# Optimization experiments

Hardware: AMD Instinct MI355X
Metric: run time of the kernel (lower is better)

Reference implementation:

```python
import jax, jax.numpy as jnp
import numpy as np

N_NODES = 100000
N_EDGES = 1600000
IN_CH = 3
HID = 32
BN_EPS = 1e-5


def setup_inputs() -> dict:
    key = jax.random.key(0)
    k_x, k_e1, k_e2, k_w, k_b, k_p = jax.random.split(key, 6)
    x = jax.random.normal(k_x, (N_NODES, IN_CH), dtype=jnp.float32)
    src = jax.random.randint(k_e1, (N_EDGES,), 0, N_NODES)
    dst = jax.random.randint(k_e2, (N_EDGES,), 0, N_NODES)
    edge_index = jnp.stack([src, dst]).astype(jnp.int64)
    # GCNConv linear params (glorot-ish init)
    W = jax.random.normal(k_w, (IN_CH, HID), dtype=jnp.float32) / np.sqrt(IN_CH)
    b = jnp.zeros((HID,), dtype=jnp.float32)
    bn_gamma = jnp.ones((HID,), dtype=jnp.float32)
    bn_beta = jnp.zeros((HID,), dtype=jnp.float32)
    prelu_w = jnp.full((1,), 0.25, dtype=jnp.float32)  # torch PReLU default
    return {"x": x, "edge_index": edge_index, "W": W, "b": b,
            "bn_gamma": bn_gamma, "bn_beta": bn_beta, "prelu_w": prelu_w}


def reference(x, edge_index, W, b, bn_gamma, bn_beta, prelu_w):
    src, dst = edge_index[0], edge_index[1]
    n = x.shape[0]
    # --- GCNConv: sym-normalized aggregation with self-loops ---
    # degree including self loop (edge weights = 1)
    deg = 1.0 + jax.ops.segment_sum(jnp.ones_like(src, dtype=x.dtype), dst,
                                    num_segments=n)
    dinv = jax.lax.rsqrt(deg)                       # deg^{-1/2}, [N]
    h = x @ W                                       # [N, HID]
    norm = dinv[src] * dinv[dst]                    # [E]
    msg = h[src] * norm[:, None]                    # [E, HID] gather
    agg = jax.ops.segment_sum(msg, dst, num_segments=n)  # scatter-add
    agg = agg + h * (1.0 / deg)[:, None]            # self-loop term
    agg = agg + b
    # --- BatchNorm1d (training-mode batch statistics, biased var) ---
    mean = jnp.mean(agg, axis=0)
    var = jnp.mean(jnp.square(agg - mean), axis=0)
    xhat = (agg - mean) * jax.lax.rsqrt(var + BN_EPS)
    y = xhat * bn_gamma + bn_beta
    # --- PReLU (single shared slope) ---
    y = jnp.where(y >= 0, y, prelu_w[0] * y)
    # dropout(p=0.5) is identity in eval / deterministic reference
    return y
```

## Files before the change

kernel.cpp:

```cpp
#include <hip/hip_runtime.h>

#define N_NODES 100000
#define N_EDGES 1600000
#define HID 32
#define BN_EPS 1e-5f

#define EPB   4096
#define NBLK  391
#define BSZ   512
#define NBUCK 196
#define SRC_MASK 0x1FFFFu


__global__ void bin_kernel(const int* __restrict__ src, const int* __restrict__ dst,
                           unsigned* __restrict__ bbuf, int* __restrict__ blen,
                           int* __restrict__ boffs) {
    __shared__ int hist[NBUCK], offs[NBUCK], curs[NBUCK];
    __shared__ int sc[256];
    __shared__ unsigned stage[EPB];
    int tid = threadIdx.x, blk = blockIdx.x;
    int e0 = blk * EPB;
    int cnt = N_EDGES - e0; if (cnt > EPB) cnt = EPB;

    unsigned pk[EPB / 256];
    int bk[EPB / 256];
#pragma unroll
    for (int i = 0; i < EPB / 256; ++i) {
        int j = tid + i * 256;
        if (j < cnt) {
            int e = e0 + j;
            int s = src[e], d = dst[e];
            bk[i] = d >> 9;
            pk[i] = ((unsigned)(d & (BSZ - 1)) << 17) | (unsigned)s;
        } else bk[i] = -1;
    }
    for (int j = tid; j < NBUCK; j += 256) hist[j] = 0;
    __syncthreads();
#pragma unroll
    for (int i = 0; i < EPB / 256; ++i)
        if (bk[i] >= 0) atomicAdd(&hist[bk[i]], 1);
    __syncthreads();
    int h = (tid < NBUCK) ? hist[tid] : 0;
    sc[tid] = h;
    __syncthreads();
    for (int off = 1; off < 256; off <<= 1) {
        int v = (tid >= off) ? sc[tid - off] : 0;
        __syncthreads();
        sc[tid] += v;
        __syncthreads();
    }
    if (tid < NBUCK) { offs[tid] = sc[tid] - h; curs[tid] = sc[tid] - h; }
    __syncthreads();
#pragma unroll
    for (int i = 0; i < EPB / 256; ++i)
        if (bk[i] >= 0) {
            int p = atomicAdd(&curs[bk[i]], 1);
            stage[p] = pk[i];
        }
    __syncthreads();
    for (int j = tid; j < cnt; j += 256) bbuf[e0 + j] = stage[j];
    for (int j = tid; j < NBUCK; j += 256) {
        blen[j * NBLK + blk]  = hist[j];
        boffs[j * NBLK + blk] = e0 + offs[j];
    }
}

__global__ void degxd_kernel(const unsigned* __restrict__ bbuf, const int* __restrict__ blen,
                             const int* __restrict__ boffs, const float* __restrict__ x,
                             float4* __restrict__ xd) {
    __shared__ int hist[BSZ];
    int tid = threadIdx.x, b = blockIdx.x;
    for (int j = tid; j < BSZ; j += 512) hist[j] = 0;
    __syncthreads();
    for (int r = tid; r < NBLK; r += 512) {
        int len = blen[b * NBLK + r];
        int off = boffs[b * NBLK + r];
        for (int k = 0; k < len; ++k) {
            unsigned p = bbuf[off + k];
            atomicAdd(&hist[p >> 17], 1);
        }
    }
    __syncthreads();
    int base = b << 9;
    for (int l = tid; l < BSZ; l += 512) {
        int n = base + l;
        if (n < N_NODES) {
            float rd = rsqrtf(1.0f + (float)hist[l]);
            xd[n] = make_float4(x[3 * n] * rd, x[3 * n + 1] * rd, x[3 * n + 2] * rd, rd);
        }
    }
}

__global__ void accum_kernel(const unsigned* __restrict__ bbuf, const int* __restrict__ blen,
                             const int* __restrict__ boffs, const float4* __restrict__ xd,
                             float4* __restrict__ S4, float* __restrict__ stats) {
    __shared__ float S[BSZ * 3];
    __shared__ float ls[8][9];
    int tid = threadIdx.x, b = blockIdx.x;
    for (int j = tid; j < BSZ * 3; j += 512) S[j] = 0.f;
    __syncthreads();
    for (int r = tid; r < NBLK; r += 512) {
        int len = blen[b * NBLK + r];
        int off = boffs[b * NBLK + r];
        for (int k = 0; k < len; ++k) {
            unsigned p = bbuf[off + k];
            float4 v = xd[p & SRC_MASK];
            int l3 = (int)(p >> 17) * 3;
            atomicAdd(&S[l3 + 0], v.x);
            atomicAdd(&S[l3 + 1], v.y);
            atomicAdd(&S[l3 + 2], v.z);
        }
    }
    __syncthreads();
    int base = b << 9;
    float st[9];
#pragma unroll
    for (int q = 0; q < 9; ++q) st[q] = 0.f;
    for (int l = tid; l < BSZ; l += 512) {
        int n = base + l;
        if (n < N_NODES) {
            float4 self = xd[n];
            float sx = S[l * 3 + 0] + self.x;
            float sy = S[l * 3 + 1] + self.y;
            float sz = S[l * 3 + 2] + self.z;
            S4[n] = make_float4(sx, sy, sz, self.w);
            float ax = self.w * sx, ay = self.w * sy, az = self.w * sz;
            st[0] += ax; st[1] += ay; st[2] += az;
            st[3] += ax * ax; st[4] += ax * ay; st[5] += ax * az;
            st[6] += ay * ay; st[7] += ay * az; st[8] += az * az;
        }
    }
    for (int m = 1; m < 64; m <<= 1)
#pragma unroll
        for (int q = 0; q < 9; ++q) st[q] += __shfl_xor(st[q], m);
    int wave = tid >> 6;
    if ((tid & 63) == 0)
#pragma unroll
        for (int q = 0; q < 9; ++q) ls[wave][q] = st[q];
    __syncthreads();
    if (tid < 9) {
        float s = 0.f;
#pragma unroll
        for (int w = 0; w < 8; ++w) s += ls[w][tid];
        atomicAdd(&stats[tid], s);
    }
}

__global__ void finalize_kernel(const float* __restrict__ stats, const float* __restrict__ W,
                                const float* __restrict__ b, const float* __restrict__ gamma,
                                const float* __restrict__ beta, float* __restrict__ cbuf) {
    int c = threadIdx.x;
    if (c >= HID) return;
    float m1x = stats[0], m1y = stats[1], m1z = stats[2];
    float Mxx = stats[3], Mxy = stats[4], Mxz = stats[5];
    float Myy = stats[6], Myz = stats[7], Mzz = stats[8];
    float w0 = W[c], w1 = W[HID + c], w2 = W[2 * HID + c];
    const float invn = 1.0f / (float)N_NODES;
    float m1w = m1x * w0 + m1y * w1 + m1z * w2;
    float mean = m1w * invn + b[c];
    float quad = w0 * w0 * Mxx + w1 * w1 * Myy + w2 * w2 * Mzz
               + 2.f * (w0 * w1 * Mxy + w0 * w2 * Mxz + w1 * w2 * Myz);
    float ex2 = quad * invn + 2.f * b[c] * m1w * invn + b[c] * b[c];
    float var = ex2 - mean * mean;
    float inv = rsqrtf(var + BN_EPS);
    float sc = gamma[c] * inv;
    float sh = beta[c] - mean * sc;
    cbuf[c] = w0 * sc;
    cbuf[HID + c] = w1 * sc;
    cbuf[2 * HID + c] = w2 * sc;
    cbuf[3 * HID + c] = b[c] * sc + sh;
}

__global__ void final_out_kernel(const float4* __restrict__ S4, const float* __restrict__ cbuf,
                                 const float* __restrict__ prelu, float* __restrict__ out) {
    int t = blockIdx.x * blockDim.x + threadIdx.x;
    if (t >= N_NODES * HID) return;
    int n = t >> 5, c = t & 31;
    float4 s = S4[n];
    float y = s.w * (s.x * cbuf[c] + s.y * cbuf[HID + c] + s.z * cbuf[2 * HID + c])
            + cbuf[3 * HID + c];
    float a = prelu[0];
    out[t] = y >= 0.f ? y : a * y;
}


__global__ void fb_count_kernel(const int* __restrict__ dst, int* __restrict__ cnt) {
    int e = blockIdx.x * blockDim.x + threadIdx.x;
    if (e < N_EDGES) atomicAdd(&cnt[dst[e]], 1);
}

__global__ void fb_xd_kernel(const float* __restrict__ x, const int* __restrict__ cnt,
                             float4* __restrict__ xd, float4* __restrict__ S4) {
    int n = blockIdx.x * blockDim.x + threadIdx.x;
    if (n >= N_NODES) return;
    float rd = rsqrtf(1.0f + (float)cnt[n]);
    float4 v = make_float4(x[3 * n] * rd, x[3 * n + 1] * rd, x[3 * n + 2] * rd, rd);
    xd[n] = v;
    S4[n] = v;
}

__global__ void fb_scatter_kernel(const int* __restrict__ src, const int* __restrict__ dst,
                                  const float4* __restrict__ xd, float4* __restrict__ S4) {
    int e = blockIdx.x * blockDim.x + threadIdx.x;
    if (e >= N_EDGES) return;
    int s = src[e], d = dst[e];
    float4 v = xd[s];
    float* p = (float*)&S4[d];
    atomicAdd(p + 0, v.x);
    atomicAdd(p + 1, v.y);
    atomicAdd(p + 2, v.z);
}

__global__ void fb_stats_kernel(const float4* __restrict__ S4, float* __restrict__ stats) {
    __shared__ float ls[4][9];
    int tid = threadIdx.x;
    int n = blockIdx.x * blockDim.x + tid;
    float st[9];
#pragma unroll
    for (int q = 0; q < 9; ++q) st[q] = 0.f;
    if (n < N_NODES) {
        float4 s = S4[n];
        float ax = s.w * s.x, ay = s.w * s.y, az = s.w * s.z;
        st[0] = ax; st[1] = ay; st[2] = az;
        st[3] = ax * ax; st[4] = ax * ay; st[5] = ax * az;
        st[6] = ay * ay; st[7] = ay * az; st[8] = az * az;
    }
    for (int m = 1; m < 64; m <<= 1)
#pragma unroll
        for (int q = 0; q < 9; ++q) st[q] += __shfl_xor(st[q], m);
    int wave = tid >> 6;
    if ((tid & 63) == 0)
#pragma unroll
        for (int q = 0; q < 9; ++q) ls[wave][q] = st[q];
    __syncthreads();
    if (tid < 9) {
        float s = ls[0][tid] + ls[1][tid] + ls[2][tid] + ls[3][tid];
        atomicAdd(&stats[tid], s);
    }
}


extern "C" void kernel_launch(void* const* d_in, const int* in_sizes, int n_in,
                              void* d_out, int out_size, void* d_ws, size_t ws_size,
                              hipStream_t stream) {
    const float* x     = (const float*)d_in[0];
    const int*   ei    = (const int*)d_in[1];
    const float* W     = (const float*)d_in[2];
    const float* b     = (const float*)d_in[3];
    const float* gamma = (const float*)d_in[4];
    const float* beta  = (const float*)d_in[5];
    const float* prelu = (const float*)d_in[6];

    const int* src = ei;
    const int* dst = ei + N_EDGES;
    char* ws = (char*)d_ws;
    float* out = (float*)d_out;

    const size_t NEEDED = 10219872;

    if (ws_size >= NEEDED) {
        float*    stats = (float*)(ws);
        float*    cbuf  = (float*)(ws + 64);
        unsigned* bbuf  = (unsigned*)(ws + 640);
        int*      blen  = (int*)(ws + 6406784);
        int*      boffs = (int*)(ws + 6713328);
        float4*   xd    = (float4*)(ws + 7019872);
        float4*   S4    = (float4*)(ws + 8619872);

        hipMemsetAsync(stats, 0, 64, stream);
        bin_kernel<<<NBLK, 256, 0, stream>>>(src, dst, bbuf, blen, boffs);
        degxd_kernel<<<NBUCK, 512, 0, stream>>>(bbuf, blen, boffs, x, xd);
        accum_kernel<<<NBUCK, 512, 0, stream>>>(bbuf, blen, boffs, xd, S4, stats);
        finalize_kernel<<<1, 64, 0, stream>>>(stats, W, b, gamma, beta, cbuf);
        final_out_kernel<<<(N_NODES * HID + 255) / 256, 256, 0, stream>>>(S4, cbuf, prelu, out);
    } else {
        int*    cnt   = (int*)(ws);
        float*  stats = (float*)(ws + 400000);
        float*  cbuf  = (float*)(ws + 400064);
        float4* xd    = (float4*)(ws + 400640);
        float4* S4    = (float4*)(ws + 2000640);

        hipMemsetAsync(ws, 0, 400064, stream);
        fb_count_kernel<<<(N_EDGES + 255) / 256, 256, 0, stream>>>(dst, cnt);
        fb_xd_kernel<<<(N_NODES + 255) / 256, 256, 0, stream>>>(x, cnt, xd, S4);
        fb_scatter_kernel<<<(N_EDGES + 255) / 256, 256, 0, stream>>>(src, dst, xd, S4);
        fb_stats_kernel<<<(N_NODES + 255) / 256, 256, 0, stream>>>(S4, stats);
        finalize_kernel<<<1, 64, 0, stream>>>(stats, W, b, gamma, beta, cbuf);
        final_out_kernel<<<(N_NODES * HID + 255) / 256, 256, 0, stream>>>(S4, cbuf, prelu, out);
    }
}
```

Before: 142.9 us.

## Split bucket degree and accumulation work across 8 blocks per bucket

The degree-count and accumulation kernels previously gave each destination bucket one 512-thread block. In that block each thread walked a whole source-block run serially, giving only 196 blocks and long sequential loops. Now each bucket is split into 8 groups of runs, with wave-per-run and lane-strided edge processing. Partial results are merged into global counts and S4 with global atomics. This adds separate xd and stats kernels plus extra global atomic traffic and launches, in exchange for much higher parallelism and coalesced bbuf reads.

Result: slower. 169.8 us (+18.8%).

```diff
diff --git a/kernel.cpp b/kernel.cpp
--- a/kernel.cpp
+++ b/kernel.cpp
@@ -10,6 +10,8 @@
 #define BSZ   512
 #define NBUCK 196
 #define SRC_MASK 0x1FFFFu
+#define GSPL  8
+#define RPB   ((NBLK + GSPL - 1) / GSPL)
 
 
 __global__ void bin_kernel(const int* __restrict__ src, const int* __restrict__ dst,
@@ -65,44 +67,57 @@
     }
 }
 
-__global__ void degxd_kernel(const unsigned* __restrict__ bbuf, const int* __restrict__ blen,
-                             const int* __restrict__ boffs, const float* __restrict__ x,
-                             float4* __restrict__ xd) {
+__global__ void deg_kernel(const unsigned* __restrict__ bbuf, const int* __restrict__ blen,
+                           const int* __restrict__ boffs, int* __restrict__ cnt) {
     __shared__ int hist[BSZ];
-    int tid = threadIdx.x, b = blockIdx.x;
-    for (int j = tid; j < BSZ; j += 512) hist[j] = 0;
-    __syncthreads();
-    for (int r = tid; r < NBLK; r += 512) {
+    int tid = threadIdx.x;
+    int b = blockIdx.x >> 3;
+    int g = blockIdx.x & 7;
+    for (int j = tid; j < BSZ; j += 256) hist[j] = 0;
+    __syncthreads();
+    int wave = tid >> 6, lane = tid & 63;
+    int r0 = g * RPB;
+    int r1 = r0 + RPB; if (r1 > NBLK) r1 = NBLK;
+    for (int r = r0 + wave; r < r1; r += 4) {
         int len = blen[b * NBLK + r];
         int off = boffs[b * NBLK + r];
-        for (int k = 0; k < len; ++k) {
-            unsigned p = bbuf[off + k];
-            atomicAdd(&hist[p >> 17], 1);
-        }
+        for (int k = lane; k < len; k += 64)
+            atomicAdd(&hist[bbuf[off + k] >> 17], 1);
     }
     __syncthreads();
     int base = b << 9;
-    for (int l = tid; l < BSZ; l += 512) {
-        int n = base + l;
-        if (n < N_NODES) {
-            float rd = rsqrtf(1.0f + (float)hist[l]);
-            xd[n] = make_float4(x[3 * n] * rd, x[3 * n + 1] * rd, x[3 * n + 2] * rd, rd);
-        }
-    }
+    for (int l = tid; l < BSZ; l += 256) {
+        int h = hist[l];
+        if (h && base + l < N_NODES) atomicAdd(&cnt[base + l], h);
+    }
+}
+
+__global__ void xd_kernel(const float* __restrict__ x, const int* __restrict__ cnt,
+                          float4* __restrict__ xd, float4* __restrict__ S4) {
+    int n = blockIdx.x * blockDim.x + threadIdx.x;
+    if (n >= N_NODES) return;
+    float rd = rsqrtf(1.0f + (float)cnt[n]);
+    float4 v = make_float4(x[3 * n] * rd, x[3 * n + 1] * rd, x[3 * n + 2] * rd, rd);
+    xd[n] = v;
+    S4[n] = v;
 }
 
 __global__ void accum_kernel(const unsigned* __restrict__ bbuf, const int* __restrict__ blen,
                              const int* __restrict__ boffs, const float4* __restrict__ xd,
-                             float4* __restrict__ S4, float* __restrict__ stats) {
+                             float4* __restrict__ S4) {
     __shared__ float S[BSZ * 3];
-    __shared__ float ls[8][9];
-    int tid = threadIdx.x, b = blockIdx.x;
-    for (int j = tid; j < BSZ * 3; j += 512) S[j] = 0.f;
-    __syncthreads();
-    for (int r = tid; r < NBLK; r += 512) {
+    int tid = threadIdx.x;
+    int b = blockIdx.x >> 3;
+    int g = blockIdx.x & 7;
+    for (int j = tid; j < BSZ * 3; j += 256) S[j] = 0.f;
+    __syncthreads();
+    int wave = tid >> 6, lane = tid & 63;
+    int r0 = g * RPB;
+    int r1 = r0 + RPB; if (r1 > NBLK) r1 = NBLK;
+    for (int r = r0 + wave; r < r1; r += 4) {
         int len = blen[b * NBLK + r];
         int off = boffs[b * NBLK + r];
-        for (int k = 0; k < len; ++k) {
+        for (int k = lane; k < len; k += 64) {
             unsigned p = bbuf[off + k];
             float4 v = xd[p & SRC_MASK];
             int l3 = (int)(p >> 17) * 3;
@@ -113,22 +128,33 @@
     }
     __syncthreads();
     int base = b << 9;
-    float st[9];
-#pragma unroll
-    for (int q = 0; q < 9; ++q) st[q] = 0.f;
-    for (int l = tid; l < BSZ; l += 512) {
+    for (int l = tid; l < BSZ; l += 256) {
         int n = base + l;
         if (n < N_NODES) {
-            float4 self = xd[n];
-            float sx = S[l * 3 + 0] + self.x;
-            float sy = S[l * 3 + 1] + self.y;
-            float sz = S[l * 3 + 2] + self.z;
-            S4[n] = make_float4(sx, sy, sz, self.w);
-            float ax = self.w * sx, ay = self.w * sy, az = self.w * sz;
-            st[0] += ax; st[1] += ay; st[2] += az;
-            st[3] += ax * ax; st[4] += ax * ay; st[5] += ax * az;
-            st[6] += ay * ay; st[7] += ay * az; st[8] += az * az;
+            float sx = S[l * 3 + 0], sy = S[l * 3 + 1], sz = S[l * 3 + 2];
+            if (sx != 0.f || sy != 0.f || sz != 0.f) {
+                float* p = (float*)&S4[n];
+                atomicAdd(p + 0, sx);
+                atomicAdd(p + 1, sy);
+                atomicAdd(p + 2, sz);
+            }
         }
+    }
+}
+
+__global__ void stats_kernel(const float4* __restrict__ S4, float* __restrict__ stats) {
+    __shared__ float ls[4][9];
+    int tid = threadIdx.x;
+    int n = blockIdx.x * blockDim.x + tid;
+    float st[9];
+#pragma unroll
+    for (int q = 0; q < 9; ++q) st[q] = 0.f;
+    if (n < N_NODES) {
+        float4 s = S4[n];
+        float ax = s.w * s.x, ay = s.w * s.y, az = s.w * s.z;
+        st[0] = ax; st[1] = ay; st[2] = az;
+        st[3] = ax * ax; st[4] = ax * ay; st[5] = ax * az;
+        st[6] = ay * ay; st[7] = ay * az; st[8] = az * az;
     }
     for (int m = 1; m < 64; m <<= 1)
 #pragma unroll
@@ -139,9 +165,7 @@
         for (int q = 0; q < 9; ++q) ls[wave][q] = st[q];
     __syncthreads();
     if (tid < 9) {
-        float s = 0.f;
-#pragma unroll
-        for (int w = 0; w < 8; ++w) s += ls[w][tid];
+        float s = ls[0][tid] + ls[1][tid] + ls[2][tid] + ls[3][tid];
         atomicAdd(&stats[tid], s);
     }
 }
@@ -189,16 +213,6 @@
     if (e < N_EDGES) atomicAdd(&cnt[dst[e]], 1);
 }
 
-__global__ void fb_xd_kernel(const float* __restrict__ x, const int* __restrict__ cnt,
-                             float4* __restrict__ xd, float4* __restrict__ S4) {
-    int n = blockIdx.x * blockDim.x + threadIdx.x;
-    if (n >= N_NODES) return;
-    float rd = rsqrtf(1.0f + (float)cnt[n]);
-    float4 v = make_float4(x[3 * n] * rd, x[3 * n + 1] * rd, x[3 * n + 2] * rd, rd);
-    xd[n] = v;
-    S4[n] = v;
-}
-
 __global__ void fb_scatter_kernel(const int* __restrict__ src, const int* __restrict__ dst,
                                   const float4* __restrict__ xd, float4* __restrict__ S4) {
     int e = blockIdx.x * blockDim.x + threadIdx.x;
@@ -211,34 +225,6 @@
     atomicAdd(p + 2, v.z);
 }
 
-__global__ void fb_stats_kernel(const float4* __restrict__ S4, float* __restrict__ stats) {
-    __shared__ float ls[4][9];
-    int tid = threadIdx.x;
-    int n = blockIdx.x * blockDim.x + tid;
-    float st[9];
-#pragma unroll
-    for (int q = 0; q < 9; ++q) st[q] = 0.f;
-    if (n < N_NODES) {
-        float4 s = S4[n];
-        float ax = s.w * s.x, ay = s.w * s.y, az = s.w * s.z;
-        st[0] = ax; st[1] = ay; st[2] = az;
-        st[3] = ax * ax; st[4] = ax * ay; st[5] = ax * az;
-        st[6] = ay * ay; st[7] = ay * az; st[8] = az * az;
-    }
-    for (int m = 1; m < 64; m <<= 1)
-#pragma unroll
-        for (int q = 0; q < 9; ++q) st[q] += __shfl_xor(st[q], m);
-    int wave = tid >> 6;
-    if ((tid & 63) == 0)
-#pragma unroll
-        for (int q = 0; q < 9; ++q) ls[wave][q] = st[q];
-    __syncthreads();
-    if (tid < 9) {
-        float s = ls[0][tid] + ls[1][tid] + ls[2][tid] + ls[3][tid];
-        atomicAdd(&stats[tid], s);
-    }
-}
-
 
 extern "C" void kernel_launch(void* const* d_in, const int* in_sizes, int n_in,
                               void* d_out, int out_size, void* d_ws, size_t ws_size,
@@ -256,21 +242,24 @@
     char* ws = (char*)d_ws;
     float* out = (float*)d_out;
 
-    const size_t NEEDED = 10219872;
+    const size_t NEEDED = 10619872;
 
     if (ws_size >= NEEDED) {
-        float*    stats = (float*)(ws);
-        float*    cbuf  = (float*)(ws + 64);
-        unsigned* bbuf  = (unsigned*)(ws + 640);
-        int*      blen  = (int*)(ws + 6406784);
-        int*      boffs = (int*)(ws + 6713328);
-        float4*   xd    = (float4*)(ws + 7019872);
-        float4*   S4    = (float4*)(ws + 8619872);
-
-        hipMemsetAsync(stats, 0, 64, stream);
+        int*      cnt   = (int*)(ws);
+        float*    stats = (float*)(ws + 400000);
+        float*    cbuf  = (float*)(ws + 400064);
+        unsigned* bbuf  = (unsigned*)(ws + 400640);
+        int*      blen  = (int*)(ws + 6806784);
+        int*      boffs = (int*)(ws + 7113328);
+        float4*   xd    = (float4*)(ws + 7419872);
+        float4*   S4    = (float4*)(ws + 9019872);
+
+        hipMemsetAsync(ws, 0, 400064, stream);
         bin_kernel<<<NBLK, 256, 0, stream>>>(src, dst, bbuf, blen, boffs);
-        degxd_kernel<<<NBUCK, 512, 0, stream>>>(bbuf, blen, boffs, x, xd);
-        accum_kernel<<<NBUCK, 512, 0, stream>>>(bbuf, blen, boffs, xd, S4, stats);
+        deg_kernel<<<NBUCK * GSPL, 256, 0, stream>>>(bbuf, blen, boffs, cnt);
+        xd_kernel<<<(N_NODES + 255) / 256, 256, 0, stream>>>(x, cnt, xd, S4);
+        accum_kernel<<<NBUCK * GSPL, 256, 0, stream>>>(bbuf, blen, boffs, xd, S4);
+        stats_kernel<<<(N_NODES + 255) / 256, 256, 0, stream>>>(S4, stats);
         finalize_kernel<<<1, 64, 0, stream>>>(stats, W, b, gamma, beta, cbuf);
         final_out_kernel<<<(N_NODES * HID + 255) / 256, 256, 0, stream>>>(S4, cbuf, prelu, out);
     } else {
@@ -282,9 +271,9 @@
 
         hipMemsetAsync(ws, 0, 400064, stream);
         fb_count_kernel<<<(N_EDGES + 255) / 256, 256, 0, stream>>>(dst, cnt);
-        fb_xd_kernel<<<(N_NODES + 255) / 256, 256, 0, stream>>>(x, cnt, xd, S4);
+        xd_kernel<<<(N_NODES + 255) / 256, 256, 0, stream>>>(x, cnt, xd, S4);
         fb_scatter_kernel<<<(N_EDGES + 255) / 256, 256, 0, stream>>>(src, dst, xd, S4);
-        fb_stats_kernel<<<(N_NODES + 255) / 256, 256, 0, stream>>>(S4, stats);
+        stats_kernel<<<(N_NODES + 255) / 256, 256, 0, stream>>>(S4, stats);
         finalize_kernel<<<1, 64, 0, stream>>>(stats, W, b, gamma, beta, cbuf);
         final_out_kernel<<<(N_NODES * HID + 255) / 256, 256, 0, stream>>>(S4, cbuf, prelu, out);
     }
```

## Compact bucketed edges into contiguous per-bucket arrays and fuse finalize into output

Applied to the files above, without the earlier changes.

Adds two prefix-scan kernels and a scatter pass that copy each destination bucket's edge runs into one contiguous array, folding the degree histogram and xd computation into that pass. The accumulate kernel then streams a contiguous range with 1024 threads instead of having each thread walk one variable-length run serially. This targets the poor parallelism and uncoalesced reads of the old per-run loops. The BN finalize is folded into a grid-stride output kernel so one launch is removed, at the cost of extra workspace, an extra copy of the edge buffer and two small scan launches.

After: 147.5 us. 3.3% more time.

```diff
diff --git a/kernel.cpp b/kernel.cpp
--- a/kernel.cpp
+++ b/kernel.cpp
@@ -13,7 +13,7 @@
 
 
 __global__ void bin_kernel(const int* __restrict__ src, const int* __restrict__ dst,
-                           unsigned* __restrict__ bbuf, int* __restrict__ blen,
+                           unsigned* __restrict__ staged, int* __restrict__ blen,
                            int* __restrict__ boffs) {
     __shared__ int hist[NBUCK], offs[NBUCK], curs[NBUCK];
     __shared__ int sc[256];
@@ -22,165 +22,203 @@
     int e0 = blk * EPB;
     int cnt = N_EDGES - e0; if (cnt > EPB) cnt = EPB;
 
-    unsigned pk[EPB / 256];
-    int bk[EPB / 256];
-#pragma unroll
-    for (int i = 0; i < EPB / 256; ++i) {
-        int j = tid + i * 256;
+    unsigned pk[8]; int bk[8];
+#pragma unroll
+    for (int i = 0; i < 8; ++i) {
+        int j = tid + i * 512;
         if (j < cnt) {
             int e = e0 + j;
-            int s = src[e], d = dst[e];
+            int d = dst[e];
             bk[i] = d >> 9;
-            pk[i] = ((unsigned)(d & (BSZ - 1)) << 17) | (unsigned)s;
+            pk[i] = ((unsigned)(d & (BSZ - 1)) << 17) | (unsigned)src[e];
         } else bk[i] = -1;
     }
-    for (int j = tid; j < NBUCK; j += 256) hist[j] = 0;
-    __syncthreads();
-#pragma unroll
-    for (int i = 0; i < EPB / 256; ++i)
+    for (int j = tid; j < NBUCK; j += 512) hist[j] = 0;
+    __syncthreads();
+#pragma unroll
+    for (int i = 0; i < 8; ++i)
         if (bk[i] >= 0) atomicAdd(&hist[bk[i]], 1);
     __syncthreads();
     int h = (tid < NBUCK) ? hist[tid] : 0;
-    sc[tid] = h;
+    if (tid < 256) sc[tid] = h;
     __syncthreads();
     for (int off = 1; off < 256; off <<= 1) {
-        int v = (tid >= off) ? sc[tid - off] : 0;
-        __syncthreads();
-        sc[tid] += v;
-        __syncthreads();
-    }
-    if (tid < NBUCK) { offs[tid] = sc[tid] - h; curs[tid] = sc[tid] - h; }
-    __syncthreads();
-#pragma unroll
-    for (int i = 0; i < EPB / 256; ++i)
+        int v = 0;
+        if (tid < 256 && tid >= off) v = sc[tid - off];
+        __syncthreads();
+        if (tid < 256) sc[tid] += v;
+        __syncthreads();
+    }
+    if (tid < NBUCK) { int ex = sc[tid] - h; offs[tid] = ex; curs[tid] = ex; }
+    __syncthreads();
+#pragma unroll
+    for (int i = 0; i < 8; ++i)
         if (bk[i] >= 0) {
             int p = atomicAdd(&curs[bk[i]], 1);
             stage[p] = pk[i];
         }
     __syncthreads();
-    for (int j = tid; j < cnt; j += 256) bbuf[e0 + j] = stage[j];
-    for (int j = tid; j < NBUCK; j += 256) {
+    for (int j = tid; j < cnt; j += 512) staged[e0 + j] = stage[j];
+    for (int j = tid; j < NBUCK; j += 512) {
         blen[j * NBLK + blk]  = hist[j];
         boffs[j * NBLK + blk] = e0 + offs[j];
     }
 }
 
-__global__ void degxd_kernel(const unsigned* __restrict__ bbuf, const int* __restrict__ blen,
-                             const int* __restrict__ boffs, const float* __restrict__ x,
-                             float4* __restrict__ xd) {
+__global__ void scan1_kernel(const int* __restrict__ blen, int* __restrict__ runoff,
+                             int* __restrict__ tot) {
+    __shared__ int sc[512];
+    int tid = threadIdx.x, b = blockIdx.x;
+    int v = (tid < NBLK) ? blen[b * NBLK + tid] : 0;
+    sc[tid] = v;
+    __syncthreads();
+    for (int off = 1; off < 512; off <<= 1) {
+        int t = (tid >= off) ? sc[tid - off] : 0;
+        __syncthreads();
+        sc[tid] += t;
+        __syncthreads();
+    }
+    if (tid < NBLK) runoff[b * NBLK + tid] = sc[tid] - v;
+    if (tid == 511) tot[b] = sc[511];
+}
+
+__global__ void scan2_kernel(const int* __restrict__ tot, int* __restrict__ bstart) {
+    __shared__ int sc[256];
+    int tid = threadIdx.x;
+    int v = (tid < NBUCK) ? tot[tid] : 0;
+    sc[tid] = v;
+    __syncthreads();
+    for (int off = 1; off < 256; off <<= 1) {
+        int t = (tid >= off) ? sc[tid - off] : 0;
+        __syncthreads();
+        sc[tid] += t;
+        __syncthreads();
+    }
+    if (tid < NBUCK) bstart[tid] = sc[tid] - v;
+    if (tid == 255) bstart[NBUCK] = sc[255];
+}
+
+__global__ void scatter2_kernel(const unsigned* __restrict__ staged, const int* __restrict__ blen,
+                                const int* __restrict__ boffs, const int* __restrict__ runoff,
+                                const int* __restrict__ bstart, const float* __restrict__ x,
+                                unsigned* __restrict__ bbuf2, float4* __restrict__ xd) {
     __shared__ int hist[BSZ];
+    __shared__ int l_len[NBLK], l_soff[NBLK], l_doff[NBLK];
     int tid = threadIdx.x, b = blockIdx.x;
-    for (int j = tid; j < BSZ; j += 512) hist[j] = 0;
-    __syncthreads();
-    for (int r = tid; r < NBLK; r += 512) {
-        int len = blen[b * NBLK + r];
-        int off = boffs[b * NBLK + r];
-        for (int k = 0; k < len; ++k) {
-            unsigned p = bbuf[off + k];
+    int bs = bstart[b];
+    for (int j = tid; j < BSZ; j += 1024) hist[j] = 0;
+    for (int j = tid; j < NBLK; j += 1024) {
+        l_len[j]  = blen[b * NBLK + j];
+        l_soff[j] = boffs[b * NBLK + j];
+        l_doff[j] = bs + runoff[b * NBLK + j];
+    }
+    __syncthreads();
+    int wv = tid >> 6, lane = tid & 63;
+    for (int r = wv; r < NBLK; r += 16) {
+        int len = l_len[r];
+        int so = l_soff[r], dof = l_doff[r];
+        for (int k = lane; k < len; k += 64) {
+            unsigned p = staged[so + k];
+            bbuf2[dof + k] = p;
             atomicAdd(&hist[p >> 17], 1);
         }
     }
     __syncthreads();
-    int base = b << 9;
-    for (int l = tid; l < BSZ; l += 512) {
-        int n = base + l;
+    if (tid < BSZ) {
+        int n = (b << 9) + tid;
         if (n < N_NODES) {
-            float rd = rsqrtf(1.0f + (float)hist[l]);
+            float rd = rsqrtf(1.0f + (float)hist[tid]);
             xd[n] = make_float4(x[3 * n] * rd, x[3 * n + 1] * rd, x[3 * n + 2] * rd, rd);
         }
     }
 }
 
-__global__ void accum_kernel(const unsigned* __restrict__ bbuf, const int* __restrict__ blen,
-                             const int* __restrict__ boffs, const float4* __restrict__ xd,
-                             float4* __restrict__ S4, float* __restrict__ stats) {
+__global__ void accum_kernel(const unsigned* __restrict__ bbuf2, const int* __restrict__ bstart,
+                             const float4* __restrict__ xd, float4* __restrict__ S4,
+                             float* __restrict__ stats) {
     __shared__ float S[BSZ * 3];
-    __shared__ float ls[8][9];
+    __shared__ float ls[16][9];
     int tid = threadIdx.x, b = blockIdx.x;
-    for (int j = tid; j < BSZ * 3; j += 512) S[j] = 0.f;
-    __syncthreads();
-    for (int r = tid; r < NBLK; r += 512) {
-        int len = blen[b * NBLK + r];
-        int off = boffs[b * NBLK + r];
-        for (int k = 0; k < len; ++k) {
-            unsigned p = bbuf[off + k];
-            float4 v = xd[p & SRC_MASK];
-            int l3 = (int)(p >> 17) * 3;
-            atomicAdd(&S[l3 + 0], v.x);
-            atomicAdd(&S[l3 + 1], v.y);
-            atomicAdd(&S[l3 + 2], v.z);
-        }
-    }
-    __syncthreads();
-    int base = b << 9;
+    for (int j = tid; j < BSZ * 3; j += 1024) S[j] = 0.f;
+    __syncthreads();
+    int e0 = bstart[b], e1 = bstart[b + 1];
+    for (int e = e0 + tid; e < e1; e += 1024) {
+        unsigned p = bbuf2[e];
+        float4 v = xd[p & SRC_MASK];
+        int l3 = (int)(p >> 17) * 3;
+        atomicAdd(&S[l3 + 0], v.x);
+        atomicAdd(&S[l3 + 1], v.y);
+        atomicAdd(&S[l3 + 2], v.z);
+    }
+    __syncthreads();
     float st[9];
 #pragma unroll
     for (int q = 0; q < 9; ++q) st[q] = 0.f;
-    for (int l = tid; l < BSZ; l += 512) {
-        int n = base + l;
+    if (tid < BSZ) {
+        int n = (b << 9) + tid;
         if (n < N_NODES) {
             float4 self = xd[n];
-            float sx = S[l * 3 + 0] + self.x;
-            float sy = S[l * 3 + 1] + self.y;
-            float sz = S[l * 3 + 2] + self.z;
+            float sx = S[tid * 3 + 0] + self.x;
+            float sy = S[tid * 3 + 1] + self.y;
+            float sz = S[tid * 3 + 2] + self.z;
             S4[n] = make_float4(sx, sy, sz, self.w);
             float ax = self.w * sx, ay = self.w * sy, az = self.w * sz;
-            st[0] += ax; st[1] += ay; st[2] += az;
-            st[3] += ax * ax; st[4] += ax * ay; st[5] += ax * az;
-            st[6] += ay * ay; st[7] += ay * az; st[8] += az * az;
+            st[0] = ax; st[1] = ay; st[2] = az;
+            st[3] = ax * ax; st[4] = ax * ay; st[5] = ax * az;
+            st[6] = ay * ay; st[7] = ay * az; st[8] = az * az;
         }
     }
     for (int m = 1; m < 64; m <<= 1)
 #pragma unroll
         for (int q = 0; q < 9; ++q) st[q] += __shfl_xor(st[q], m);
-    int wave = tid >> 6;
+    int wv = tid >> 6;
     if ((tid & 63) == 0)
 #pragma unroll
-        for (int q = 0; q < 9; ++q) ls[wave][q] = st[q];
+        for (int q = 0; q < 9; ++q) ls[wv][q] = st[q];
     __syncthreads();
     if (tid < 9) {
         float s = 0.f;
 #pragma unroll
-        for (int w = 0; w < 8; ++w) s += ls[w][tid];
+        for (int w = 0; w < 16; ++w) s += ls[w][tid];
         atomicAdd(&stats[tid], s);
     }
 }
 
-__global__ void finalize_kernel(const float* __restrict__ stats, const float* __restrict__ W,
-                                const float* __restrict__ b, const float* __restrict__ gamma,
-                                const float* __restrict__ beta, float* __restrict__ cbuf) {
-    int c = threadIdx.x;
-    if (c >= HID) return;
-    float m1x = stats[0], m1y = stats[1], m1z = stats[2];
-    float Mxx = stats[3], Mxy = stats[4], Mxz = stats[5];
-    float Myy = stats[6], Myz = stats[7], Mzz = stats[8];
-    float w0 = W[c], w1 = W[HID + c], w2 = W[2 * HID + c];
-    const float invn = 1.0f / (float)N_NODES;
-    float m1w = m1x * w0 + m1y * w1 + m1z * w2;
-    float mean = m1w * invn + b[c];
-    float quad = w0 * w0 * Mxx + w1 * w1 * Myy + w2 * w2 * Mzz
-               + 2.f * (w0 * w1 * Mxy + w0 * w2 * Mxz + w1 * w2 * Myz);
-    float ex2 = quad * invn + 2.f * b[c] * m1w * invn + b[c] * b[c];
-    float var = ex2 - mean * mean;
-    float inv = rsqrtf(var + BN_EPS);
-    float sc = gamma[c] * inv;
-    float sh = beta[c] - mean * sc;
-    cbuf[c] = w0 * sc;
-    cbuf[HID + c] = w1 * sc;
-    cbuf[2 * HID + c] = w2 * sc;
-    cbuf[3 * HID + c] = b[c] * sc + sh;
-}
-
-__global__ void final_out_kernel(const float4* __restrict__ S4, const float* __restrict__ cbuf,
+__global__ void final_out_kernel(const float4* __restrict__ S4, const float* __restrict__ stats,
+                                 const float* __restrict__ W, const float* __restrict__ bb,
+                                 const float* __restrict__ gamma, const float* __restrict__ beta,
                                  const float* __restrict__ prelu, float* __restrict__ out) {
-    int t = blockIdx.x * blockDim.x + threadIdx.x;
-    if (t >= N_NODES * HID) return;
-    int n = t >> 5, c = t & 31;
-    float4 s = S4[n];
-    float y = s.w * (s.x * cbuf[c] + s.y * cbuf[HID + c] + s.z * cbuf[2 * HID + c])
-            + cbuf[3 * HID + c];
+    __shared__ float cb[4 * HID];
+    int tid = threadIdx.x;
+    if (tid < HID) {
+        int c = tid;
+        float m1x = stats[0], m1y = stats[1], m1z = stats[2];
+        float Mxx = stats[3], Mxy = stats[4], Mxz = stats[5];
+        float Myy = stats[6], Myz = stats[7], Mzz = stats[8];
+        float w0 = W[c], w1 = W[HID + c], w2 = W[2 * HID + c];
+        const float invn = 1.0f / (float)N_NODES;
+        float m1w = m1x * w0 + m1y * w1 + m1z * w2;
+        float mean = m1w * invn + bb[c];
+        float quad = w0 * w0 * Mxx + w1 * w1 * Myy + w2 * w2 * Mzz
+                   + 2.f * (w0 * w1 * Mxy + w0 * w2 * Mxz + w1 * w2 * Myz);
+        float ex2 = quad * invn + 2.f * bb[c] * m1w * invn + bb[c] * bb[c];
+        float var = ex2 - mean * mean;
+        float sc = gamma[c] * rsqrtf(var + BN_EPS);
+        cb[c] = w0 * sc;
+        cb[HID + c] = w1 * sc;
+        cb[2 * HID + c] = w2 * sc;
+        cb[3 * HID + c] = bb[c] * sc + (beta[c] - mean * sc);
+    }
+    __syncthreads();
     float a = prelu[0];
-    out[t] = y >= 0.f ? y : a * y;
+    int stride = gridDim.x * blockDim.x;
+    for (int t = blockIdx.x * blockDim.x + tid; t < N_NODES * HID; t += stride) {
+        int n = t >> 5, c = t & 31;
+        float4 s = S4[n];
+        float y = s.w * (s.x * cb[c] + s.y * cb[HID + c] + s.z * cb[2 * HID + c])
+                + cb[3 * HID + c];
+        out[t] = y >= 0.f ? y : a * y;
+    }
 }
 
 
@@ -228,10 +266,10 @@
     for (int m = 1; m < 64; m <<= 1)
 #pragma unroll
         for (int q = 0; q < 9; ++q) st[q] += __shfl_xor(st[q], m);
-    int wave = tid >> 6;
+    int wv = tid >> 6;
     if ((tid & 63) == 0)
 #pragma unroll
-        for (int q = 0; q < 9; ++q) ls[wave][q] = st[q];
+        for (int q = 0; q < 9; ++q) ls[wv][q] = st[q];
     __syncthreads();
     if (tid < 9) {
         float s = ls[0][tid] + ls[1][tid] + ls[2][tid] + ls[3][tid];
@@ -256,27 +294,31 @@
     char* ws = (char*)d_ws;
     float* out = (float*)d_out;
 
-    const size_t NEEDED = 10219872;
+    const size_t NEEDED = 16927456;
 
     if (ws_size >= NEEDED) {
-        float*    stats = (float*)(ws);
-        float*    cbuf  = (float*)(ws + 64);
-        unsigned* bbuf  = (unsigned*)(ws + 640);
-        int*      blen  = (int*)(ws + 6406784);
-        int*      boffs = (int*)(ws + 6713328);
-        float4*   xd    = (float4*)(ws + 7019872);
-        float4*   S4    = (float4*)(ws + 8619872);
+        float*    stats  = (float*)(ws);
+        int*      tot    = (int*)(ws + 64);
+        int*      bstart = (int*)(ws + 848);
+        int*      blen   = (int*)(ws + 1664);
+        int*      boffs  = (int*)(ws + 308208);
+        int*      runoff = (int*)(ws + 614752);
+        unsigned* staged = (unsigned*)(ws + 921312);
+        unsigned* bbuf2  = (unsigned*)(ws + 7327456);
+        float4*   xd     = (float4*)(ws + 13727456);
+        float4*   S4     = (float4*)(ws + 15327456);
 
         hipMemsetAsync(stats, 0, 64, stream);
-        bin_kernel<<<NBLK, 256, 0, stream>>>(src, dst, bbuf, blen, boffs);
-        degxd_kernel<<<NBUCK, 512, 0, stream>>>(bbuf, blen, boffs, x, xd);
-        accum_kernel<<<NBUCK, 512, 0, stream>>>(bbuf, blen, boffs, xd, S4, stats);
-        finalize_kernel<<<1, 64, 0, stream>>>(stats, W, b, gamma, beta, cbuf);
-        final_out_kernel<<<(N_NODES * HID + 255) / 256, 256, 0, stream>>>(S4, cbuf, prelu, out);
+        bin_kernel<<<NBLK, 512, 0, stream>>>(src, dst, staged, blen, boffs);
+        scan1_kernel<<<NBUCK, 512, 0, stream>>>(blen, runoff, tot);
+        scan2_kernel<<<1, 256, 0, stream>>>(tot, bstart);
+        scatter2_kernel<<<NBUCK, 1024, 0, stream>>>(staged, blen, boffs, runoff, bstart,
+                                                    x, bbuf2, xd);
+        accum_kernel<<<NBUCK, 1024, 0, stream>>>(bbuf2, bstart, xd, S4, stats);
+        final_out_kernel<<<2048, 256, 0, stream>>>(S4, stats, W, b, gamma, beta, prelu, out);
     } else {
         int*    cnt   = (int*)(ws);
         float*  stats = (float*)(ws + 400000);
-        float*  cbuf  = (float*)(ws + 400064);
         float4* xd    = (float4*)(ws + 400640);
         float4* S4    = (float4*)(ws + 2000640);
 
@@ -285,7 +327,6 @@
         fb_xd_kernel<<<(N_NODES + 255) / 256, 256, 0, stream>>>(x, cnt, xd, S4);
         fb_scatter_kernel<<<(N_EDGES + 255) / 256, 256, 0, stream>>>(src, dst, xd, S4);
         fb_stats_kernel<<<(N_NODES + 255) / 256, 256, 0, stream>>>(S4, stats);
-        finalize_kernel<<<1, 64, 0, stream>>>(stats, W, b, gamma, beta, cbuf);
-        final_out_kernel<<<(N_NODES * HID + 255) / 256, 256, 0, stream>>>(S4, cbuf, prelu, out);
-    }
-}
+        final_out_kernel<<<2048, 256, 0, stream>>>(S4, stats, W, b, gamma, beta, prelu, out);
+    }
+}
```
